# Performance work log

Measured on AMD Instinct MI355X. Metric: run time of the kernel, lower is better.

## Reference

```python
import jax, jax.numpy as jnp
import numpy as np

N_HEADS = 8
EPS = 1e-08


def setup_inputs() -> dict:
    key = jax.random.key(0)
    ks = jax.random.split(key, 6)
    B, T1, T2, C = 8, 2048, 512, 512
    query = jax.random.normal(ks[0], (B, T1, C), dtype=jnp.float32)
    memory = jax.random.normal(ks[1], (B, T2, C), dtype=jnp.float32)
    query_mask = jnp.ones((B, T1), dtype=bool)
    memory_mask = jnp.ones((B, T2), dtype=bool)
    attn_prior = jax.random.uniform(ks[2], (B, T1, T2), dtype=jnp.float32)
    s = 1.0 / np.sqrt(C)
    Wq = jax.random.normal(ks[3], (C, C), dtype=jnp.float32) * s
    Wkv = jax.random.normal(ks[4], (C, 2 * C), dtype=jnp.float32) * s
    Wo = jax.random.normal(ks[5], (C, C), dtype=jnp.float32) * s
    return {"query": query, "query_mask": query_mask, "memory": memory,
            "memory_mask": memory_mask, "attn_prior": attn_prior,
            "Wq": Wq, "Wkv": Wkv, "Wo": Wo}


def reference(query, query_mask, memory, memory_mask, attn_prior, Wq, Wkv, Wo):
    B, T1, C = query.shape
    T2 = memory.shape[1]
    H = N_HEADS
    Dh = C // H
    scale = Dh ** (-0.5)

    # projections (no bias, as in NeMo q_net/kv_net/o_net)
    q = (query @ Wq).reshape(B, T1, H, Dh).transpose(0, 2, 1, 3)       # (B,H,T1,Dh)
    kv = memory @ Wkv                                                    # (B,T2,2C)
    k, v = jnp.split(kv, 2, axis=-1)
    k = k.reshape(B, T2, H, Dh).transpose(0, 2, 1, 3)                    # (B,H,T2,Dh)
    v = v.reshape(B, T2, H, Dh).transpose(0, 2, 1, 3)                    # (B,H,T2,Dh)

    attn_score = jnp.einsum('bhqd,bhkd->bhqk', q, k) * scale            # (B,H,T1,T2)
    mask = memory_mask[:, None, None, :]                                 # (B,1,1,T2)
    attn_score = jnp.where(mask, attn_score, -jnp.inf)

    # log-prior fusion: log_softmax(scores) + log(prior), renormalized via softmax
    log_prior = jnp.log(attn_prior + EPS)[:, None]                       # (B,1,T1,T2)
    attn_score_log = jax.nn.log_softmax(attn_score, axis=-1) + log_prior
    attn_prob = jax.nn.softmax(attn_score_log, axis=-1)
    attn_prob = jnp.where(mask, attn_prob, 0.0)

    y = jnp.einsum('bhqk,bhkd->bqhd', attn_prob, v).reshape(B, T1, C)
    out = y @ Wo
    return out, attn_prob, attn_score
```

## Files before the change

### kernel.cpp

```cpp
#include <hip/hip_runtime.h>
#include <hip/hip_bf16.h>

#define DEV static __device__ __forceinline__

typedef __attribute__((ext_vector_type(8))) short short8;
typedef __attribute__((ext_vector_type(4))) float f32x4;
typedef __attribute__((ext_vector_type(4))) float float4v;
typedef __attribute__((ext_vector_type(4))) unsigned int uint4v;
typedef __attribute__((ext_vector_type(2))) unsigned int uint2v;


DEV unsigned short f2bf(float f) {
  union { float f; unsigned u; } x{f};
  return (unsigned short)((x.u + 0x7fffu + ((x.u >> 16) & 1u)) >> 16);
}

DEV unsigned pack_bf(float lo, float hi) {
  return (unsigned)f2bf(lo) | ((unsigned)f2bf(hi) << 16);
}

DEV float fast_exp2(float x) { return __builtin_amdgcn_exp2f(x); }
DEV float fast_log2(float x) { return __builtin_amdgcn_logf(x); }

DEV f32x4 mfma16(short8 a, short8 b, f32x4 c) {
  return __builtin_amdgcn_mfma_f32_16x16x32_bf16(a, b, c, 0, 0, 0);
}

DEV void gload16(const void* g, void* l) {
  __builtin_amdgcn_global_load_lds(
      (const __attribute__((address_space(1))) unsigned*)g,
      (__attribute__((address_space(3))) unsigned*)l, 16, 0, 0);
}

__global__ __launch_bounds__(256) void transpose_cvt(
    const float* __restrict__ src, unsigned short* __restrict__ dst, int Ndim) {
  __shared__ float tile[32][33];
  const int k0 = blockIdx.x * 32;
  const int n0 = blockIdx.y * 32;
  const int tx = threadIdx.x & 31, ty = threadIdx.x >> 5;
#pragma unroll
  for (int i = 0; i < 4; ++i)
    tile[ty + i * 8][tx] = src[(size_t)(k0 + ty + i * 8) * Ndim + n0 + tx];
  __syncthreads();
#pragma unroll
  for (int i = 0; i < 4; ++i)
    dst[(size_t)(n0 + ty + i * 8) * 512 + k0 + tx] = f2bf(tile[tx][ty + i * 8]);
}

template <int MODE>
__global__ __launch_bounds__(256, 2) void gemm_kernel(
    const void* __restrict__ Aptr, const unsigned short* __restrict__ WT,
    void* __restrict__ out0, void* __restrict__ out1) {
  __shared__ char smemA[16384];
  __shared__ char smemB[16384];
  const int tid = threadIdx.x;
  const int w = tid >> 6, l = tid & 63, c = l & 15, g = l >> 4;
  const int wm = w >> 1, wn = w & 1;
  const int row0 = blockIdx.x * 128, col0 = blockIdx.y * 128;

  f32x4 acc[4][4];
#pragma unroll
  for (int m = 0; m < 4; ++m)
#pragma unroll
    for (int n = 0; n < 4; ++n) acc[m][n] = f32x4{0.f, 0.f, 0.f, 0.f};

  for (int kt = 0; kt < 8; ++kt) {
    if (MODE != 2) {
      const int arow = tid >> 1, ahalf = tid & 1;
      const float* asrc =
          (const float*)Aptr + (size_t)(row0 + arow) * 512 + kt * 64 + ahalf * 32;
      float4v av[8];
#pragma unroll
      for (int i = 0; i < 8; ++i) av[i] = *(const float4v*)(asrc + i * 4);
#pragma unroll
      for (int qq = 0; qq < 4; ++qq) {
        uint4v pk;
        pk.x = pack_bf(av[2 * qq][0], av[2 * qq][1]);
        pk.y = pack_bf(av[2 * qq][2], av[2 * qq][3]);
        pk.z = pack_bf(av[2 * qq + 1][0], av[2 * qq + 1][1]);
        pk.w = pack_bf(av[2 * qq + 1][2], av[2 * qq + 1][3]);
        int off = (arow * 128 + ahalf * 64 + qq * 16) ^ ((arow & 7) << 4);
        *(uint4v*)(smemA + off) = pk;
      }
    } else {
#pragma unroll
      for (int cc = 0; cc < 4; ++cc) {
        int o = cc * 4096 + tid * 16;
        int r_ = o >> 7;
        gload16((const char*)Aptr + (size_t)(row0 + r_) * 1024 + kt * 128 +
                    ((o ^ ((r_ & 7) << 4)) & 127),
                smemA + o);
      }
    }
#pragma unroll
    for (int cc = 0; cc < 4; ++cc) {
      int o = cc * 4096 + tid * 16;
      int r_ = o >> 7;
      gload16((const char*)WT + (size_t)(col0 + r_) * 1024 + kt * 128 +
                  ((o ^ ((r_ & 7) << 4)) & 127),
              smemB + o);
    }
    __syncthreads();
#pragma unroll
    for (int s = 0; s < 2; ++s) {
      short8 af[4], bfr[4];
#pragma unroll
      for (int m = 0; m < 4; ++m) {
        int row = wm * 64 + m * 16 + c;
        af[m] = *(const short8*)(smemA +
                                 ((row * 128 + g * 16 + s * 64) ^ ((row & 7) << 4)));
      }
#pragma unroll
      for (int n = 0; n < 4; ++n) {
        int row = wn * 64 + n * 16 + c;
        bfr[n] = *(const short8*)(smemB +
                                  ((row * 128 + g * 16 + s * 64) ^ ((row & 7) << 4)));
      }
#pragma unroll
      for (int m = 0; m < 4; ++m)
#pragma unroll
        for (int n = 0; n < 4; ++n) acc[m][n] = mfma16(af[m], bfr[n], acc[m][n]);
    }
    __syncthreads();
  }

#pragma unroll
  for (int m = 0; m < 4; ++m)
#pragma unroll
    for (int n = 0; n < 4; ++n)
#pragma unroll
      for (int r = 0; r < 4; ++r) {
        float v = acc[m][n][r];
        int grow = row0 + wm * 64 + m * 16 + g * 4 + r;
        int gcol = col0 + wn * 64 + n * 16 + c;
        if (MODE == 0) {
          int bb = grow >> 11, q = grow & 2047, hh = gcol >> 6, d = gcol & 63;
          ((unsigned short*)out0)[(((size_t)bb * 8 + hh) * 2048 + q) * 64 + d] =
              f2bf(v * 0.125f);
        } else if (MODE == 1) {
          int bb = grow >> 9, t2 = grow & 511;
          if (gcol < 512) {
            int hh = gcol >> 6, d = gcol & 63;
            ((unsigned short*)out0)[(((size_t)bb * 8 + hh) * 512 + t2) * 64 + d] =
                f2bf(v);
          } else {
            int hh = (gcol - 512) >> 6, d = gcol & 63;
            ((unsigned short*)out1)[(((size_t)bb * 8 + hh) * 64 + d) * 512 + t2] =
                f2bf(v);
          }
        } else {
          ((float*)out0)[(size_t)grow * 512 + gcol] = v;
        }
      }
}

__global__ __launch_bounds__(256, 1) void attn_kernel(
    const unsigned short* __restrict__ Qb, const unsigned short* __restrict__ Kb,
    const unsigned short* __restrict__ VTb, const float* __restrict__ prior,
    float* __restrict__ score, float* __restrict__ prob,
    unsigned short* __restrict__ yb) {
  extern __shared__ char smem[];
  char* smemP = smem + 65536;
  const int tid = threadIdx.x;
  const int w = tid >> 6, l = tid & 63;
  const int c = l & 15, g = l >> 4;
  const int bh = blockIdx.x >> 5, qt = blockIdx.x & 31;
  const int b = bh >> 3, h = bh & 7;
  const int q0 = qt * 64;

  const char* kbase = (const char*)(Kb + (size_t)bh * 512 * 64);
#pragma unroll
  for (int cc = 0; cc < 16; ++cc) {
    int o = cc * 4096 + tid * 16;
    gload16(kbase + (o ^ (((o >> 7) & 7) << 4)), smem + o);
  }

  const char* qbase = (const char*)(Qb + ((size_t)bh * 2048 + q0 + w * 16) * 64);
  short8 qf0 = *(const short8*)(qbase + c * 128 + g * 16);
  short8 qf1 = *(const short8*)(qbase + c * 128 + g * 16 + 64);

  f32x4 acc[32];
#pragma unroll
  for (int n = 0; n < 32; ++n) acc[n] = f32x4{0.f, 0.f, 0.f, 0.f};

  __syncthreads();

#pragma unroll
  for (int n = 0; n < 32; ++n) {
    int row = n * 16 + c;
    int base = row * 128 + g * 16;
    short8 kf0 = *(const short8*)(smem + (base ^ ((row & 7) << 4)));
    short8 kf1 = *(const short8*)(smem + ((base + 64) ^ ((row & 7) << 4)));
    acc[n] = mfma16(kf0, qf0, acc[n]);
    acc[n] = mfma16(kf1, qf1, acc[n]);
  }

  __syncthreads();

  const char* vbase = (const char*)(VTb + (size_t)bh * 64 * 512);
#pragma unroll
  for (int cc = 0; cc < 16; ++cc) {
    int o = cc * 4096 + tid * 16;
    gload16(vbase + (o ^ (((o >> 10) & 7) << 4)), smem + o);
  }

  const int q = q0 + w * 16 + c;
  float* sb = score + ((size_t)bh * 2048 + q) * 512 + g * 4;
  float* pb = prob + ((size_t)bh * 2048 + q) * 512 + g * 4;
  const float* prb = prior + ((size_t)b * 2048 + q) * 512 + g * 4;

  float rsum = 0.f;
#pragma unroll
  for (int n = 0; n < 32; ++n) {
    *(float4v*)(sb + n * 16) = acc[n];
    float4v p4 = *(const float4v*)(prb + n * 16);
    f32x4 e;
#pragma unroll
    for (int r = 0; r < 4; ++r) {
      float t = acc[n][r] * 1.44269504f + fast_log2(p4[r] + 1e-8f);
      e[r] = fast_exp2(t);
    }
    rsum += (e[0] + e[1]) + (e[2] + e[3]);
    acc[n] = e;
  }
  rsum += __shfl_xor(rsum, 16);
  rsum += __shfl_xor(rsum, 32);
  const float rs = 1.f / rsum;

  char* pw = smemP + w * 16384;
#pragma unroll
  for (int n = 0; n < 32; ++n) {
    f32x4 p = acc[n];
    p[0] *= rs; p[1] *= rs; p[2] *= rs; p[3] *= rs;
    *(float4v*)(pb + n * 16) = p;
    uint2v u;
    u.x = pack_bf(p[0], p[1]);
    u.y = pack_bf(p[2], p[3]);
    int off = (c * 1024 + n * 32 + g * 8) ^ ((c & 7) << 4);
    *(uint2v*)(pw + off) = u;
  }

  __syncthreads();

  f32x4 yacc[4];
#pragma unroll
  for (int t = 0; t < 4; ++t) yacc[t] = f32x4{0.f, 0.f, 0.f, 0.f};
#pragma unroll
  for (int s = 0; s < 16; ++s) {
    short8 pf =
        *(const short8*)(pw + ((c * 1024 + g * 16 + s * 64) ^ ((c & 7) << 4)));
#pragma unroll
    for (int nt = 0; nt < 4; ++nt) {
      int vrow = nt * 16 + c;
      short8 vf = *(const short8*)(smem +
                                   ((vrow * 1024 + g * 16 + s * 64) ^ ((vrow & 7) << 4)));
      yacc[nt] = mfma16(pf, vf, yacc[nt]);
    }
  }
  unsigned short* yb_ =
      yb + ((size_t)b * 2048 + q0 + w * 16) * 512 + h * 64;
#pragma unroll
  for (int nt = 0; nt < 4; ++nt)
#pragma unroll
    for (int r = 0; r < 4; ++r)
      yb_[(g * 4 + r) * 512 + nt * 16 + c] = f2bf(yacc[nt][r]);
}


extern "C" void kernel_launch(void* const* d_in, const int* in_sizes, int n_in,
                              void* d_out, int out_size, void* d_ws, size_t ws_size,
                              hipStream_t stream) {
  (void)in_sizes; (void)n_in; (void)out_size;
  const float* query = (const float*)d_in[0];
  const float* memory = (const float*)d_in[2];
  const float* prior = (const float*)d_in[4];
  const float* Wq = (const float*)d_in[5];
  const float* Wkv = (const float*)d_in[6];
  const float* Wo = (const float*)d_in[7];

  float* out = (float*)d_out;
  float* prob = out + (size_t)8 * 2048 * 512;
  float* score = prob + (size_t)64 * 2048 * 512;

  char* ws = (char*)d_ws;
  size_t off = 0;
  unsigned short* WqT = (unsigned short*)(ws + off);  off += (size_t)512 * 512 * 2;
  unsigned short* WkvT = (unsigned short*)(ws + off); off += (size_t)1024 * 512 * 2;
  unsigned short* WoT = (unsigned short*)(ws + off);  off += (size_t)512 * 512 * 2;
  unsigned short* Qb = (unsigned short*)(ws + off);   off += (size_t)64 * 2048 * 64 * 2;
  unsigned short* Kb = (unsigned short*)(ws + off);   off += (size_t)64 * 512 * 64 * 2;
  unsigned short* VT = (unsigned short*)(ws + off);   off += (size_t)64 * 64 * 512 * 2;
  unsigned short* yb = (unsigned short*)(ws + off);   off += (size_t)8 * 2048 * 512 * 2;
  if (ws_size < off) return;

  (void)hipFuncSetAttribute((const void*)attn_kernel,
                            hipFuncAttributeMaxDynamicSharedMemorySize, 131072);

  transpose_cvt<<<dim3(16, 16), 256, 0, stream>>>(Wq, WqT, 512);
  transpose_cvt<<<dim3(16, 32), 256, 0, stream>>>(Wkv, WkvT, 1024);
  transpose_cvt<<<dim3(16, 16), 256, 0, stream>>>(Wo, WoT, 512);
  gemm_kernel<0><<<dim3(128, 4), 256, 0, stream>>>(query, WqT, Qb, nullptr);
  gemm_kernel<1><<<dim3(32, 8), 256, 0, stream>>>(memory, WkvT, Kb, VT);
  attn_kernel<<<2048, 256, 131072, stream>>>(Qb, Kb, VT, prior, score, prob, yb);
  gemm_kernel<2><<<dim3(128, 4), 256, 0, stream>>>(yb, WoT, out, nullptr);
}
```

Baseline: 253.1 us.

## Pipeline attention over T2 tiles with double-buffered K/V and deferred normalization

Restructures the attention kernel to process keys in four 128-wide tiles, double-buffering K and V in shared memory so global loads overlap compute. The PV matmul now runs on unnormalized exponentials per tile, and the row normalization is applied to y at the end. This cuts LDS use from 128KB to 80KB so two blocks fit per CU. It also remaps block indices so heads sharing a prior tile are adjacent for L2 reuse, and it uses nontemporal stores for the large score, prob and output writes. The cost is more barriers, and P is rounded to bf16 before normalization rather than after.

Result: faster. 229.4 us (-9.4%).

```diff
diff --git a/kernel.cpp b/kernel.cpp
--- a/kernel.cpp
+++ b/kernel.cpp
@@ -149,121 +149,144 @@
                 f2bf(v);
           }
         } else {
-          ((float*)out0)[(size_t)grow * 512 + gcol] = v;
+          __builtin_nontemporal_store(
+              v, (float*)out0 + (size_t)grow * 512 + gcol);
         }
       }
 }
 
-__global__ __launch_bounds__(256, 1) void attn_kernel(
+__global__ __launch_bounds__(256, 2) void attn_kernel(
     const unsigned short* __restrict__ Qb, const unsigned short* __restrict__ Kb,
     const unsigned short* __restrict__ VTb, const float* __restrict__ prior,
     float* __restrict__ score, float* __restrict__ prob,
     unsigned short* __restrict__ yb) {
   extern __shared__ char smem[];
-  char* smemP = smem + 65536;
+  char* kl[2] = {smem, smem + 16384};
+  char* vl[2] = {smem + 32768, smem + 49152};
   const int tid = threadIdx.x;
   const int w = tid >> 6, l = tid & 63;
   const int c = l & 15, g = l >> 4;
-  const int bh = blockIdx.x >> 5, qt = blockIdx.x & 31;
-  const int b = bh >> 3, h = bh & 7;
+  char* pw = smem + 65536 + w * 4096;
+
+  const int xid = (blockIdx.x & 7) * 256 + (blockIdx.x >> 3);
+  const int h = xid & 7, qt = (xid >> 3) & 31, b = xid >> 8;
+  const int bh = b * 8 + h;
   const int q0 = qt * 64;
 
   const char* kbase = (const char*)(Kb + (size_t)bh * 512 * 64);
-#pragma unroll
-  for (int cc = 0; cc < 16; ++cc) {
-    int o = cc * 4096 + tid * 16;
-    gload16(kbase + (o ^ (((o >> 7) & 7) << 4)), smem + o);
-  }
+  const char* vbase = (const char*)(VTb + (size_t)bh * 64 * 512);
+
+  auto stageK = [&](int t, char* dst) {
+    const char* src = kbase + (size_t)t * 16384;
+#pragma unroll
+    for (int i = 0; i < 4; ++i) {
+      int o = i * 4096 + tid * 16;
+      int row = o >> 7;
+      gload16(src + row * 128 + ((o & 127) ^ ((row & 7) << 4)), dst + o);
+    }
+  };
+  auto stageV = [&](int t, char* dst) {
+#pragma unroll
+    for (int i = 0; i < 4; ++i) {
+      int o = i * 4096 + tid * 16;
+      int row = o >> 8;
+      gload16(vbase + row * 1024 + t * 256 + ((o & 255) ^ ((row & 7) << 4)),
+              dst + o);
+    }
+  };
+
+  stageK(0, kl[0]);
+  stageV(0, vl[0]);
 
   const char* qbase = (const char*)(Qb + ((size_t)bh * 2048 + q0 + w * 16) * 64);
   short8 qf0 = *(const short8*)(qbase + c * 128 + g * 16);
   short8 qf1 = *(const short8*)(qbase + c * 128 + g * 16 + 64);
-
-  f32x4 acc[32];
-#pragma unroll
-  for (int n = 0; n < 32; ++n) acc[n] = f32x4{0.f, 0.f, 0.f, 0.f};
-
-  __syncthreads();
-
-#pragma unroll
-  for (int n = 0; n < 32; ++n) {
-    int row = n * 16 + c;
-    int base = row * 128 + g * 16;
-    short8 kf0 = *(const short8*)(smem + (base ^ ((row & 7) << 4)));
-    short8 kf1 = *(const short8*)(smem + ((base + 64) ^ ((row & 7) << 4)));
-    acc[n] = mfma16(kf0, qf0, acc[n]);
-    acc[n] = mfma16(kf1, qf1, acc[n]);
-  }
-
-  __syncthreads();
-
-  const char* vbase = (const char*)(VTb + (size_t)bh * 64 * 512);
-#pragma unroll
-  for (int cc = 0; cc < 16; ++cc) {
-    int o = cc * 4096 + tid * 16;
-    gload16(vbase + (o ^ (((o >> 10) & 7) << 4)), smem + o);
-  }
 
   const int q = q0 + w * 16 + c;
   float* sb = score + ((size_t)bh * 2048 + q) * 512 + g * 4;
   float* pb = prob + ((size_t)bh * 2048 + q) * 512 + g * 4;
   const float* prb = prior + ((size_t)b * 2048 + q) * 512 + g * 4;
 
+  f32x4 acc[32];
+#pragma unroll
+  for (int n = 0; n < 32; ++n) acc[n] = f32x4{0.f, 0.f, 0.f, 0.f};
+  f32x4 yacc[4];
+#pragma unroll
+  for (int n = 0; n < 4; ++n) yacc[n] = f32x4{0.f, 0.f, 0.f, 0.f};
   float rsum = 0.f;
-#pragma unroll
-  for (int n = 0; n < 32; ++n) {
-    *(float4v*)(sb + n * 16) = acc[n];
-    float4v p4 = *(const float4v*)(prb + n * 16);
-    f32x4 e;
-#pragma unroll
-    for (int r = 0; r < 4; ++r) {
-      float t = acc[n][r] * 1.44269504f + fast_log2(p4[r] + 1e-8f);
-      e[r] = fast_exp2(t);
-    }
-    rsum += (e[0] + e[1]) + (e[2] + e[3]);
-    acc[n] = e;
+
+  __syncthreads();
+
+#pragma unroll
+  for (int t = 0; t < 4; ++t) {
+    const int cur = t & 1;
+    if (t < 3) {
+      stageK(t + 1, kl[cur ^ 1]);
+      stageV(t + 1, vl[cur ^ 1]);
+    }
+#pragma unroll
+    for (int n = 0; n < 8; ++n) {
+      const int a = t * 8 + n;
+      const int krow = n * 16 + c;
+      const int base = krow * 128 + g * 16;
+      short8 kf0 = *(const short8*)(kl[cur] + (base ^ ((krow & 7) << 4)));
+      short8 kf1 = *(const short8*)(kl[cur] + ((base + 64) ^ ((krow & 7) << 4)));
+      acc[a] = mfma16(kf0, qf0, acc[a]);
+      acc[a] = mfma16(kf1, qf1, acc[a]);
+    }
+#pragma unroll
+    for (int n = 0; n < 8; ++n) {
+      const int a = t * 8 + n;
+      __builtin_nontemporal_store((float4v)acc[a],
+                                  (float4v*)(sb + t * 128 + n * 16));
+      float4v p4 = *(const float4v*)(prb + t * 128 + n * 16);
+      f32x4 e;
+#pragma unroll
+      for (int r = 0; r < 4; ++r)
+        e[r] = fast_exp2(acc[a][r] * 1.44269504f + fast_log2(p4[r] + 1e-8f));
+      rsum += (e[0] + e[1]) + (e[2] + e[3]);
+      acc[a] = e;
+      uint2v u;
+      u.x = pack_bf(e[0], e[1]);
+      u.y = pack_bf(e[2], e[3]);
+      *(uint2v*)(pw + ((c * 256 + n * 32 + g * 8) ^ ((c & 7) << 4))) = u;
+    }
+#pragma unroll
+    for (int s = 0; s < 4; ++s) {
+      short8 pf =
+          *(const short8*)(pw + ((c * 256 + s * 64 + g * 16) ^ ((c & 7) << 4)));
+#pragma unroll
+      for (int nt = 0; nt < 4; ++nt) {
+        const int vrow = nt * 16 + c;
+        short8 vf = *(const short8*)(
+            vl[cur] + ((vrow * 256 + s * 64 + g * 16) ^ ((vrow & 7) << 4)));
+        yacc[nt] = mfma16(pf, vf, yacc[nt]);
+      }
+    }
+    __syncthreads();
   }
+
   rsum += __shfl_xor(rsum, 16);
   rsum += __shfl_xor(rsum, 32);
   const float rs = 1.f / rsum;
 
-  char* pw = smemP + w * 16384;
-#pragma unroll
+  #pragma unroll
   for (int n = 0; n < 32; ++n) {
-    f32x4 p = acc[n];
-    p[0] *= rs; p[1] *= rs; p[2] *= rs; p[3] *= rs;
-    *(float4v*)(pb + n * 16) = p;
-    uint2v u;
-    u.x = pack_bf(p[0], p[1]);
-    u.y = pack_bf(p[2], p[3]);
-    int off = (c * 1024 + n * 32 + g * 8) ^ ((c & 7) << 4);
-    *(uint2v*)(pw + off) = u;
+    float4v p;
+#pragma unroll
+    for (int r = 0; r < 4; ++r) p[r] = acc[n][r] * rs;
+    __builtin_nontemporal_store(p, (float4v*)(pb + n * 16));
   }
 
-  __syncthreads();
-
-  f32x4 yacc[4];
-#pragma unroll
-  for (int t = 0; t < 4; ++t) yacc[t] = f32x4{0.f, 0.f, 0.f, 0.f};
-#pragma unroll
-  for (int s = 0; s < 16; ++s) {
-    short8 pf =
-        *(const short8*)(pw + ((c * 1024 + g * 16 + s * 64) ^ ((c & 7) << 4)));
-#pragma unroll
-    for (int nt = 0; nt < 4; ++nt) {
-      int vrow = nt * 16 + c;
-      short8 vf = *(const short8*)(smem +
-                                   ((vrow * 1024 + g * 16 + s * 64) ^ ((vrow & 7) << 4)));
-      yacc[nt] = mfma16(pf, vf, yacc[nt]);
-    }
-  }
-  unsigned short* yb_ =
-      yb + ((size_t)b * 2048 + q0 + w * 16) * 512 + h * 64;
+  float rsq[4];
+#pragma unroll
+  for (int r = 0; r < 4; ++r) rsq[r] = __shfl(rs, g * 4 + r);
+  unsigned short* yb_ = yb + ((size_t)b * 2048 + q0 + w * 16) * 512 + h * 64;
 #pragma unroll
   for (int nt = 0; nt < 4; ++nt)
 #pragma unroll
     for (int r = 0; r < 4; ++r)
-      yb_[(g * 4 + r) * 512 + nt * 16 + c] = f2bf(yacc[nt][r]);
+      yb_[(g * 4 + r) * 512 + nt * 16 + c] = f2bf(yacc[nt][r] * rsq[r]);
 }
 
 
@@ -294,13 +317,13 @@
   if (ws_size < off) return;
 
   (void)hipFuncSetAttribute((const void*)attn_kernel,
-                            hipFuncAttributeMaxDynamicSharedMemorySize, 131072);
+                            hipFuncAttributeMaxDynamicSharedMemorySize, 81920);
 
   transpose_cvt<<<dim3(16, 16), 256, 0, stream>>>(Wq, WqT, 512);
   transpose_cvt<<<dim3(16, 32), 256, 0, stream>>>(Wkv, WkvT, 1024);
   transpose_cvt<<<dim3(16, 16), 256, 0, stream>>>(Wo, WoT, 512);
   gemm_kernel<0><<<dim3(128, 4), 256, 0, stream>>>(query, WqT, Qb, nullptr);
   gemm_kernel<1><<<dim3(32, 8), 256, 0, stream>>>(memory, WkvT, Kb, VT);
-  attn_kernel<<<2048, 256, 131072, stream>>>(Qb, Kb, VT, prior, score, prob, yb);
+  attn_kernel<<<2048, 256, 81920, stream>>>(Qb, Kb, VT, prior, score, prob, yb);
   gemm_kernel<2><<<dim3(128, 4), 256, 0, stream>>>(yb, WoT, out, nullptr);
 }
```
